# Kernel tuning notes

Hardware: AMD Instinct MI355X
Metric: run time of the kernel (lower is better)

Reference implementation:

```python
import jax, jax.numpy as jnp
import numpy as np

UNITS = 256
IN_DIM = 256
OUT_DIM = 10
TOL = 1e-4
MAX_ITER = 50


def setup_inputs() -> dict:
    key = jax.random.key(0)
    ks = jax.random.split(key, 16)
    B = 65536
    s = 1.0 / np.sqrt(UNITS)
    inp = {
        "x": jax.random.normal(ks[0], (B, IN_DIM), dtype=jnp.float32),
        "w_in": jax.random.normal(ks[1], (IN_DIM, UNITS), dtype=jnp.float32) * s,
        "b_in": jax.random.normal(ks[2], (UNITS,), dtype=jnp.float32) * 0.01,
        "w_out": jax.random.normal(ks[3], (UNITS, OUT_DIM), dtype=jnp.float32) * s,
        "b_out": jax.random.normal(ks[4], (OUT_DIM,), dtype=jnp.float32) * 0.01,
    }
    eye = jnp.eye(UNITS, dtype=jnp.float32)
    for i in range(4):
        # well-conditioned (invertible) implicit-layer weight: I + small perturbation
        inp[f"w{i+1}"] = eye + 0.1 * jax.random.normal(ks[5 + 2 * i], (UNITS, UNITS), dtype=jnp.float32) * s
        inp[f"b{i+1}"] = jax.random.normal(ks[6 + 2 * i], (UNITS,), dtype=jnp.float32) * 0.01
    return inp


def newton_block(x, W, b):
    # Solve z @ W = x + tanh(x) + b by Newton iteration with early exit on ||g||.
    c = x + jnp.tanh(x) + b  # [B, n]
    z0 = x
    g0 = z0 @ W - c

    def cond(state):
        z, g, it = state
        return (it < MAX_ITER) & (jnp.linalg.norm(g) >= TOL)

    def body(state):
        z, g, it = state
        # torch.solve(g[:, :, None], W^T.repeat(B,1,1)): shared matrix -> one solve
        z = z - jnp.linalg.solve(W.T, g.T).T
        g = z @ W - c
        return (z, g, it + 1)

    z, _, _ = jax.lax.while_loop(cond, body, (z0, g0, jnp.asarray(0)))
    z = jax.lax.stop_gradient(z)  # torch loop runs under no_grad
    # final differentiable correction (torch: z = z - (z@W - x - tanh(x) - b))
    return z - (z @ W - c)


def reference(x, w_in, b_in, w1, b1, w2, b2, w3, b3, w4, b4, w_out, b_out):
    z = x @ w_in + b_in
    z = newton_block(z, w1, b1)
    z = newton_block(z, w2, b2)
    z = newton_block(z, w3, b3)
    z = newton_block(z, w4, b4)
    logits = z @ w_out + b_out
    return jax.nn.softmax(logits, axis=1)
```

## Files before the change

kernel.cpp:

```cpp
#include <hip/hip_runtime.h>
#include <hip/hip_fp16.h>
#include <math.h>


typedef __attribute__((ext_vector_type(8))) short short8;
typedef __attribute__((ext_vector_type(4))) float f32x4;

__device__ __forceinline__ float tanh_fast(float x) {
#if __has_builtin(__builtin_amdgcn_exp2f)
  float e = __builtin_amdgcn_exp2f(x * 2.8853900817779268f);
#else
  float e = __expf(2.0f * x);
#endif
  return 1.0f - 2.0f * __builtin_amdgcn_rcpf(e + 1.0f);
}
__device__ __forceinline__ unsigned rn_pair16(float v0, float v1) {
  __half2 h = __floats2half2_rn(v0, v1);
  return *reinterpret_cast<unsigned*>(&h);
}
__device__ __forceinline__ unsigned rtz_pair16(float v0, float v1) {
#if __has_builtin(__builtin_amdgcn_cvt_pkrtz)
  typedef __fp16 h2v __attribute__((ext_vector_type(2)));
  h2v h = __builtin_amdgcn_cvt_pkrtz(v0, v1);
  return *reinterpret_cast<unsigned*>(&h);
#else
  return rn_pair16(v0, v1);
#endif
}

__global__ __launch_bounds__(256) void ns_poly_k(
    const float* __restrict__ w1, const float* __restrict__ w2,
    const float* __restrict__ w3, const float* __restrict__ w4,
    const float* __restrict__ w_in, const float* __restrict__ w_out,
    unsigned* __restrict__ pk) {
  const int bid = blockIdx.x;
  const int t = threadIdx.x;
  if (bid >= 256) {
    int idx = (bid - 256) * 256 + t;
    {
      int kc = idx >> 12;
      int nt = (idx >> 8) & 15;
      int lane = (idx >> 2) & 63;
      int d = idx & 3;
      int n = nt * 16 + (lane & 15);
      int kb = kc * 32 + (lane >> 4) * 8 + d * 2;
      pk[idx] = rn_pair16(w_in[kb * 256 + n], w_in[(kb + 1) * 256 + n]);
    }
    int idx2 = idx + 32768;
    if (idx2 < 34816) {
      int r2 = idx2 - 32768;
      int kc = r2 >> 8;
      int lane = (r2 >> 2) & 63;
      int d = r2 & 3;
      int n = lane & 15;
      int kb = kc * 32 + (lane >> 4) * 8 + d * 2;
      float v0 = (n < 10) ? w_out[kb * 10 + n] : 0.0f;
      float v1 = (n < 10) ? w_out[(kb + 1) * 10 + n] : 0.0f;
      pk[5 * 32768 + r2] = rn_pair16(v0, v1);
    }
    return;
  }
  const int m = bid >> 6;
  const int r0 = (bid & 63) * 4;
  const float* __restrict__ W = (m == 0) ? w1 : (m == 1) ? w2 : (m == 2) ? w3 : w4;
  __shared__ float S[4][256];

#pragma unroll
  for (int i = 0; i < 4; ++i) {
    int e = i * 256 + t;
    int r = e >> 8, c = e & 255;
    S[r][c] = (((r0 + r) == c) ? 6.0f : 0.0f) - W[(r0 + r) * 256 + c];
  }
  __syncthreads();

  const float coef[4] = {-15.0f, 20.0f, -15.0f, 6.0f};
#pragma unroll
  for (int step = 0; step < 4; ++step) {
    float acc[4];
#pragma unroll
    for (int r = 0; r < 4; ++r) acc[r] = 0.0f;
    for (int k = 0; k < 256; k += 4) {
      float4 sv[4];
#pragma unroll
      for (int r = 0; r < 4; ++r) sv[r] = *(const float4*)&S[r][k];
      float wv0 = W[(k + 0) * 256 + t];
      float wv1 = W[(k + 1) * 256 + t];
      float wv2 = W[(k + 2) * 256 + t];
      float wv3 = W[(k + 3) * 256 + t];
#pragma unroll
      for (int r = 0; r < 4; ++r) {
        acc[r] = fmaf(sv[r].x, wv0, acc[r]);
        acc[r] = fmaf(sv[r].y, wv1, acc[r]);
        acc[r] = fmaf(sv[r].z, wv2, acc[r]);
        acc[r] = fmaf(sv[r].w, wv3, acc[r]);
      }
    }
    __syncthreads();
    float cdiag = coef[step];
#pragma unroll
    for (int r = 0; r < 4; ++r)
      S[r][t] = acc[r] + (((r0 + r) == t) ? cdiag : 0.0f);
    __syncthreads();
  }

  const int kc = r0 >> 5;
  const int quad = (r0 >> 3) & 3;
  const int d0 = (r0 & 7) >> 1;
#pragma unroll
  for (int i = 0; i < 2; ++i) {
    int q = i * 256 + t;
    int nt = q >> 5;
    int n16 = (q >> 1) & 15;
    int dd = q & 1;
    int n = nt * 16 + n16;
    int lane = quad * 16 + n16;
    unsigned word = rn_pair16(S[2 * dd][n], S[2 * dd + 1][n]);
    pk[(m + 1) * 32768 + kc * 4096 + nt * 256 + lane * 4 + (d0 + dd)] = word;
  }
}

template <int MT>
__global__ __launch_bounds__(256, 4) void fused_k(
    const float* __restrict__ x, const unsigned* __restrict__ pk,
    const float* __restrict__ b_in,
    const float* __restrict__ b1, const float* __restrict__ b2,
    const float* __restrict__ b3, const float* __restrict__ b4,
    const float* __restrict__ b_out, float* __restrict__ out) {
  constexpr int NR = MT * 16;
  __shared__ unsigned short zpl[NR * 256];
  const int t = threadIdx.x;
  const int ln = t & 63;
  const int wv = t >> 6;
  const int quad = ln >> 4;
  const int n16 = ln & 15;
  const int grow0 = blockIdx.x * NR;

#pragma unroll
  for (int i = 0; i < MT * 4; ++i) {
    int e = i * 1024 + t * 4;
    int r = e >> 8, c = e & 255;
    float4 v = *(const float4*)(x + (grow0 + r) * 256 + c);
    int idx = r * 256 + (((c >> 3) ^ (r & 31)) * 8) + (c & 7);
    uint2 zp;
    zp.x = rtz_pair16(v.x, v.y);
    zp.y = rtz_pair16(v.z, v.w);
    *(uint2*)&zpl[idx] = zp;
  }
  __syncthreads();

  const float* bnv[4] = {b1, b2, b3, b4};
  f32x4 acc[MT][4];

  for (int layer = 0; layer < 5; ++layer) {
    const unsigned* pkl = pk + layer * 32768 + wv * 1024 + ln * 4;
#pragma unroll
    for (int mt = 0; mt < MT; ++mt)
#pragma unroll
      for (int nt = 0; nt < 4; ++nt) acc[mt][nt] = (f32x4){0.f, 0.f, 0.f, 0.f};

#pragma unroll 2
    for (int kc = 0; kc < 8; ++kc) {
      short8 wh[4], zf[MT];
      const unsigned* pb = pkl + kc * 4096;
#pragma unroll
      for (int nt = 0; nt < 4; ++nt) wh[nt] = *(const short8*)(pb + nt * 256);
#pragma unroll
      for (int mt = 0; mt < MT; ++mt) {
        int mm = mt * 16 + n16;
        int idx = mm * 256 + (((kc * 4 + quad) ^ (mm & 31)) * 8);
        zf[mt] = *(const short8*)&zpl[idx];
      }
#pragma unroll
      for (int mt = 0; mt < MT; ++mt)
#pragma unroll
        for (int nt = 0; nt < 4; ++nt)
          acc[mt][nt] = __builtin_amdgcn_mfma_f32_16x16x32_f16(wh[nt], zf[mt], acc[mt][nt], 0, 0, 0);
    }
    __syncthreads();

#pragma unroll
    for (int nt = 0; nt < 4; ++nt) {
      int colb = wv * 64 + nt * 16 + quad * 4;
      float4 bi = make_float4(0.f, 0.f, 0.f, 0.f);
      float4 bn4 = bi;
      if (layer == 0) bi = *(const float4*)(b_in + colb);
      if (layer < 4) bn4 = *(const float4*)(bnv[layer] + colb);
#pragma unroll
      for (int mt = 0; mt < MT; ++mt) {
        int row = mt * 16 + n16;
        float v0 = acc[mt][nt][0] + bi.x;
        float v1 = acc[mt][nt][1] + bi.y;
        float v2 = acc[mt][nt][2] + bi.z;
        float v3 = acc[mt][nt][3] + bi.w;
        if (layer < 4) {
          v0 = v0 + tanh_fast(v0) + bn4.x;
          v1 = v1 + tanh_fast(v1) + bn4.y;
          v2 = v2 + tanh_fast(v2) + bn4.z;
          v3 = v3 + tanh_fast(v3) + bn4.w;
        }
        int idx = row * 256 + (((colb >> 3) ^ (row & 31)) * 8) + (colb & 7);
        uint2 zp;
        zp.x = rtz_pair16(v0, v1);
        zp.y = rtz_pair16(v2, v3);
        *(uint2*)&zpl[idx] = zp;
      }
    }
    __syncthreads();
  }

  f32x4 lacc[MT];
#pragma unroll
  for (int mt = 0; mt < MT; ++mt) lacc[mt] = (f32x4){0.f, 0.f, 0.f, 0.f};
  const unsigned* pw = pk + 5 * 32768 + ln * 4;
#pragma unroll
  for (int kk = 0; kk < 2; ++kk) {
    int kc = wv * 2 + kk;
    short8 wh = *(const short8*)(pw + kc * 256);
#pragma unroll
    for (int mt = 0; mt < MT; ++mt) {
      int mm = mt * 16 + n16;
      int idx = mm * 256 + (((kc * 4 + quad) ^ (mm & 31)) * 8);
      short8 zf = *(const short8*)&zpl[idx];
      lacc[mt] = __builtin_amdgcn_mfma_f32_16x16x32_f16(wh, zf, lacc[mt], 0, 0, 0);
    }
  }
  __syncthreads();
  float* pbuf = (float*)zpl;
#pragma unroll
  for (int mt = 0; mt < MT; ++mt) {
    int addr = wv * (NR * 16) + (mt * 16 + n16) * 16 + quad * 4;
    *(f32x4*)&pbuf[addr] = lacc[mt];
  }
  __syncthreads();
  if (t < NR) {
    int r = t;
    float lg[10];
    float mx = -1e30f;
#pragma unroll
    for (int j = 0; j < 10; ++j) {
      float s = b_out[j];
#pragma unroll
      for (int w2 = 0; w2 < 4; ++w2) s += pbuf[w2 * (NR * 16) + r * 16 + j];
      lg[j] = s;
      mx = fmaxf(mx, s);
    }
    float sum = 0.f;
#pragma unroll
    for (int j = 0; j < 10; ++j) {
      lg[j] = __expf(lg[j] - mx);
      sum += lg[j];
    }
    float inv = 1.0f / sum;
    float* op = out + (grow0 + r) * 10;
#pragma unroll
    for (int j = 0; j < 10; ++j) op[j] = lg[j] * inv;
  }
}

extern "C" void kernel_launch(void* const* d_in, const int* in_sizes, int n_in,
                              void* d_out, int out_size, void* d_ws, size_t ws_size,
                              hipStream_t stream) {
  const float* x     = (const float*)d_in[0];
  const float* w_in  = (const float*)d_in[1];
  const float* b_in  = (const float*)d_in[2];
  const float* w_out = (const float*)d_in[3];
  const float* b_out = (const float*)d_in[4];
  const float* w1 = (const float*)d_in[5];
  const float* b1 = (const float*)d_in[6];
  const float* w2 = (const float*)d_in[7];
  const float* b2 = (const float*)d_in[8];
  const float* w3 = (const float*)d_in[9];
  const float* b3 = (const float*)d_in[10];
  const float* w4 = (const float*)d_in[11];
  const float* b4 = (const float*)d_in[12];
  float* out = (float*)d_out;

  unsigned* pk = (unsigned*)d_ws;

  ns_poly_k<<<384, 256, 0, stream>>>(w1, w2, w3, w4, w_in, w_out, pk);
  fused_k<4><<<1024, 256, 0, stream>>>(x, pk, b_in, b1, b2, b3, b4, b_out, out);
}
```

Before: 184.8 us.

## Restructure fused kernel into 1024-thread blocks with ping-pong MFMA/epilogue overlap

The fused kernel now uses 1024-thread blocks that each own 256 rows, split into four 64-row groups in shared memory. Each wave keeps its 16-column slice of the layer weights in registers (8 short8) instead of reloading weights every k-chunk. The work is software-pipelined: the tanh/bias epilogue of one row group is interleaved with the MFMA phase of the next, using two accumulator sets, so the matrix and vector units can overlap. Shared memory grows to 128 KB per block and there are fewer, larger blocks (256), which may reduce occupancy and raise register pressure.

Result: slower. 212.9 us (+15.2%).

```diff
diff --git a/kernel.cpp b/kernel.cpp
--- a/kernel.cpp
+++ b/kernel.cpp
@@ -119,141 +119,168 @@
   }
 }
 
-template <int MT>
-__global__ __launch_bounds__(256, 4) void fused_k(
+#define MFMA_PHASE(ACC, S)                                                     \
+  {                                                                            \
+    const unsigned short* pl = zpl + (S) * 16384;                              \
+    _Pragma("unroll") for (int mt = 0; mt < 4; ++mt)                           \
+        ACC[mt] = (f32x4){0.f, 0.f, 0.f, 0.f};                                 \
+    _Pragma("unroll") for (int kc = 0; kc < 8; ++kc) {                         \
+      short8 zf[4];                                                            \
+      _Pragma("unroll") for (int mt = 0; mt < 4; ++mt)                         \
+          zf[mt] = *(const short8*)&pl[rd_base[mt] + ((rd_pm[mt] ^ (kc * 4)) * 8)]; \
+      _Pragma("unroll") for (int mt = 0; mt < 4; ++mt)                         \
+          ACC[mt] = __builtin_amdgcn_mfma_f32_16x16x32_f16(wreg[kc], zf[mt],   \
+                                                           ACC[mt], 0, 0, 0); \
+    }                                                                          \
+  }
+
+#define EPI_PHASE(ACC, S, BN, BI, DOTANH)                                      \
+  {                                                                            \
+    unsigned short* pl = zpl + (S) * 16384;                                    \
+    float4 bn4 = make_float4(0.f, 0.f, 0.f, 0.f);                              \
+    float4 bi4 = make_float4(0.f, 0.f, 0.f, 0.f);                              \
+    if (DOTANH) bn4 = *(const float4*)((BN) + colb);                           \
+    if ((BI) != nullptr) bi4 = *(const float4*)((BI) + colb);                  \
+    _Pragma("unroll") for (int mt = 0; mt < 4; ++mt) {                         \
+      float v0 = ACC[mt][0] + bi4.x;                                           \
+      float v1 = ACC[mt][1] + bi4.y;                                           \
+      float v2 = ACC[mt][2] + bi4.z;                                           \
+      float v3 = ACC[mt][3] + bi4.w;                                           \
+      if (DOTANH) {                                                            \
+        v0 = v0 + tanh_fast(v0) + bn4.x;                                       \
+        v1 = v1 + tanh_fast(v1) + bn4.y;                                       \
+        v2 = v2 + tanh_fast(v2) + bn4.z;                                       \
+        v3 = v3 + tanh_fast(v3) + bn4.w;                                       \
+      }                                                                        \
+      uint2 zp;                                                                \
+      zp.x = rtz_pair16(v0, v1);                                               \
+      zp.y = rtz_pair16(v2, v3);                                               \
+      *(uint2*)&pl[wr_off[mt]] = zp;                                           \
+    }                                                                          \
+  }
+
+__global__ __launch_bounds__(1024, 4) void fused2_k(
     const float* __restrict__ x, const unsigned* __restrict__ pk,
     const float* __restrict__ b_in,
     const float* __restrict__ b1, const float* __restrict__ b2,
     const float* __restrict__ b3, const float* __restrict__ b4,
     const float* __restrict__ b_out, float* __restrict__ out) {
-  constexpr int NR = MT * 16;
-  __shared__ unsigned short zpl[NR * 256];
+  __shared__ unsigned short zpl[4 * 64 * 256];
   const int t = threadIdx.x;
   const int ln = t & 63;
   const int wv = t >> 6;
   const int quad = ln >> 4;
   const int n16 = ln & 15;
-  const int grow0 = blockIdx.x * NR;
-
-#pragma unroll
-  for (int i = 0; i < MT * 4; ++i) {
-    int e = i * 1024 + t * 4;
+  const int grow0 = blockIdx.x * 256;
+
+#pragma unroll
+  for (int i = 0; i < 16; ++i) {
+    int e = i * 4096 + t * 4;
     int r = e >> 8, c = e & 255;
     float4 v = *(const float4*)(x + (grow0 + r) * 256 + c);
-    int idx = r * 256 + (((c >> 3) ^ (r & 31)) * 8) + (c & 7);
+    int g = r >> 6, rl = r & 63;
+    int idx = g * 16384 + rl * 256 + (((c >> 3) ^ (rl & 31)) * 8) + (c & 7);
     uint2 zp;
     zp.x = rtz_pair16(v.x, v.y);
     zp.y = rtz_pair16(v.z, v.w);
     *(uint2*)&zpl[idx] = zp;
   }
+
+  const int colb = wv * 16 + quad * 4;
+  int rd_base[4], rd_pm[4], wr_off[4];
+#pragma unroll
+  for (int mt = 0; mt < 4; ++mt) {
+    int mm = mt * 16 + n16;
+    rd_base[mt] = mm * 256;
+    rd_pm[mt] = quad ^ (mm & 31);
+    wr_off[mt] = mm * 256 + (((colb >> 3) ^ (mm & 31)) * 8) + (colb & 7);
+  }
+
   __syncthreads();
 
-  const float* bnv[4] = {b1, b2, b3, b4};
-  f32x4 acc[MT][4];
+  f32x4 accA[4], accB[4];
 
   for (int layer = 0; layer < 5; ++layer) {
-    const unsigned* pkl = pk + layer * 32768 + wv * 1024 + ln * 4;
-#pragma unroll
-    for (int mt = 0; mt < MT; ++mt)
-#pragma unroll
-      for (int nt = 0; nt < 4; ++nt) acc[mt][nt] = (f32x4){0.f, 0.f, 0.f, 0.f};
-
-#pragma unroll 2
-    for (int kc = 0; kc < 8; ++kc) {
-      short8 wh[4], zf[MT];
-      const unsigned* pb = pkl + kc * 4096;
-#pragma unroll
-      for (int nt = 0; nt < 4; ++nt) wh[nt] = *(const short8*)(pb + nt * 256);
-#pragma unroll
-      for (int mt = 0; mt < MT; ++mt) {
-        int mm = mt * 16 + n16;
-        int idx = mm * 256 + (((kc * 4 + quad) ^ (mm & 31)) * 8);
-        zf[mt] = *(const short8*)&zpl[idx];
+    const unsigned* pkl = pk + layer * 32768 + wv * 256 + ln * 4;
+    short8 wreg[8];
+#pragma unroll
+    for (int kc = 0; kc < 8; ++kc) wreg[kc] = *(const short8*)(pkl + kc * 4096);
+
+    if (layer > 0) {
+      const float* bnp = (layer == 1) ? b1 : (layer == 2) ? b2 : (layer == 3) ? b3 : b4;
+      const float* bip = (layer == 1) ? b_in : nullptr;
+      EPI_PHASE(accB, 3, bnp, bip, true);
+    }
+    MFMA_PHASE(accA, 0);
+    __syncthreads();
+
+    const float* bn = (layer == 0) ? b1 : (layer == 1) ? b2 : (layer == 2) ? b3 : b4;
+    const float* bi0 = (layer == 0) ? b_in : nullptr;
+    const bool dt = (layer < 4);
+
+    EPI_PHASE(accA, 0, bn, bi0, dt);
+    MFMA_PHASE(accB, 1);
+    __syncthreads();
+    EPI_PHASE(accB, 1, bn, bi0, dt);
+    MFMA_PHASE(accA, 2);
+    __syncthreads();
+    EPI_PHASE(accA, 2, bn, bi0, dt);
+    MFMA_PHASE(accB, 3);
+    __syncthreads();
+  }
+  EPI_PHASE(accB, 3, (const float*)nullptr, (const float*)nullptr, false);
+  __syncthreads();
+
+  {
+    const int g = wv >> 2;
+    const int kw = wv & 3;
+    f32x4 lacc[4];
+#pragma unroll
+    for (int mt = 0; mt < 4; ++mt) lacc[mt] = (f32x4){0.f, 0.f, 0.f, 0.f};
+    const unsigned* pw = pk + 5 * 32768 + ln * 4;
+    const unsigned short* pl = zpl + g * 16384;
+#pragma unroll
+    for (int kk = 0; kk < 2; ++kk) {
+      int kc = kw * 2 + kk;
+      short8 wh = *(const short8*)(pw + kc * 256);
+#pragma unroll
+      for (int mt = 0; mt < 4; ++mt) {
+        short8 zf = *(const short8*)&pl[rd_base[mt] + ((rd_pm[mt] ^ (kc * 4)) * 8)];
+        lacc[mt] = __builtin_amdgcn_mfma_f32_16x16x32_f16(wh, zf, lacc[mt], 0, 0, 0);
       }
-#pragma unroll
-      for (int mt = 0; mt < MT; ++mt)
-#pragma unroll
-        for (int nt = 0; nt < 4; ++nt)
-          acc[mt][nt] = __builtin_amdgcn_mfma_f32_16x16x32_f16(wh[nt], zf[mt], acc[mt][nt], 0, 0, 0);
-    }
-    __syncthreads();
-
-#pragma unroll
-    for (int nt = 0; nt < 4; ++nt) {
-      int colb = wv * 64 + nt * 16 + quad * 4;
-      float4 bi = make_float4(0.f, 0.f, 0.f, 0.f);
-      float4 bn4 = bi;
-      if (layer == 0) bi = *(const float4*)(b_in + colb);
-      if (layer < 4) bn4 = *(const float4*)(bnv[layer] + colb);
-#pragma unroll
-      for (int mt = 0; mt < MT; ++mt) {
-        int row = mt * 16 + n16;
-        float v0 = acc[mt][nt][0] + bi.x;
-        float v1 = acc[mt][nt][1] + bi.y;
-        float v2 = acc[mt][nt][2] + bi.z;
-        float v3 = acc[mt][nt][3] + bi.w;
-        if (layer < 4) {
-          v0 = v0 + tanh_fast(v0) + bn4.x;
-          v1 = v1 + tanh_fast(v1) + bn4.y;
-          v2 = v2 + tanh_fast(v2) + bn4.z;
-          v3 = v3 + tanh_fast(v3) + bn4.w;
-        }
-        int idx = row * 256 + (((colb >> 3) ^ (row & 31)) * 8) + (colb & 7);
-        uint2 zp;
-        zp.x = rtz_pair16(v0, v1);
-        zp.y = rtz_pair16(v2, v3);
-        *(uint2*)&zpl[idx] = zp;
+    }
+    __syncthreads();
+    float* pbuf = (float*)zpl;
+#pragma unroll
+    for (int mt = 0; mt < 4; ++mt) {
+      int addr = g * 4096 + kw * 1024 + (mt * 16 + n16) * 16 + quad * 4;
+      *(f32x4*)&pbuf[addr] = lacc[mt];
+    }
+    __syncthreads();
+    if (t < 256) {
+      int g2 = t >> 6;
+      int rl = t & 63;
+      float lg[10];
+      float mx = -1e30f;
+#pragma unroll
+      for (int j = 0; j < 10; ++j) {
+        float s = b_out[j];
+#pragma unroll
+        for (int k2 = 0; k2 < 4; ++k2) s += pbuf[g2 * 4096 + k2 * 1024 + rl * 16 + j];
+        lg[j] = s;
+        mx = fmaxf(mx, s);
       }
-    }
-    __syncthreads();
-  }
-
-  f32x4 lacc[MT];
-#pragma unroll
-  for (int mt = 0; mt < MT; ++mt) lacc[mt] = (f32x4){0.f, 0.f, 0.f, 0.f};
-  const unsigned* pw = pk + 5 * 32768 + ln * 4;
-#pragma unroll
-  for (int kk = 0; kk < 2; ++kk) {
-    int kc = wv * 2 + kk;
-    short8 wh = *(const short8*)(pw + kc * 256);
-#pragma unroll
-    for (int mt = 0; mt < MT; ++mt) {
-      int mm = mt * 16 + n16;
-      int idx = mm * 256 + (((kc * 4 + quad) ^ (mm & 31)) * 8);
-      short8 zf = *(const short8*)&zpl[idx];
-      lacc[mt] = __builtin_amdgcn_mfma_f32_16x16x32_f16(wh, zf, lacc[mt], 0, 0, 0);
-    }
-  }
-  __syncthreads();
-  float* pbuf = (float*)zpl;
-#pragma unroll
-  for (int mt = 0; mt < MT; ++mt) {
-    int addr = wv * (NR * 16) + (mt * 16 + n16) * 16 + quad * 4;
-    *(f32x4*)&pbuf[addr] = lacc[mt];
-  }
-  __syncthreads();
-  if (t < NR) {
-    int r = t;
-    float lg[10];
-    float mx = -1e30f;
-#pragma unroll
-    for (int j = 0; j < 10; ++j) {
-      float s = b_out[j];
-#pragma unroll
-      for (int w2 = 0; w2 < 4; ++w2) s += pbuf[w2 * (NR * 16) + r * 16 + j];
-      lg[j] = s;
-      mx = fmaxf(mx, s);
-    }
-    float sum = 0.f;
-#pragma unroll
-    for (int j = 0; j < 10; ++j) {
-      lg[j] = __expf(lg[j] - mx);
-      sum += lg[j];
-    }
-    float inv = 1.0f / sum;
-    float* op = out + (grow0 + r) * 10;
-#pragma unroll
-    for (int j = 0; j < 10; ++j) op[j] = lg[j] * inv;
+      float sum = 0.f;
+#pragma unroll
+      for (int j = 0; j < 10; ++j) {
+        lg[j] = __expf(lg[j] - mx);
+        sum += lg[j];
+      }
+      float inv = 1.0f / sum;
+      float* op = out + (grow0 + t) * 10;
+#pragma unroll
+      for (int j = 0; j < 10; ++j) op[j] = lg[j] * inv;
+    }
   }
 }
 
@@ -278,5 +305,5 @@
   unsigned* pk = (unsigned*)d_ws;
 
   ns_poly_k<<<384, 256, 0, stream>>>(w1, w2, w3, w4, w_in, w_out, pk);
-  fused_k<4><<<1024, 256, 0, stream>>>(x, pk, b_in, b1, b2, b3, b4, b_out, out);
-}
+  fused2_k<<<256, 1024, 0, stream>>>(x, pk, b_in, b1, b2, b3, b4, b_out, out);
+}
```

## Double-buffer weight fragment loads across k-chunks and layers with MFMA priority

Applied to the files above, without the earlier changes.

Replaces the k-loop with a fully unrolled sequence that prefetches the next k-chunk's weight fragments into a second register buffer while MFMAs consume the current one. The first chunk of the next layer is also loaded before the epilogue and the initial x staging. Sched barriers pin the ordering, and s_setprio raises wave priority around the MFMA bursts. The goal is to hide global/L2 weight-load latency behind matrix math, at the cost of extra VGPRs under the 4-blocks-per-SM launch bound. The macros hardcode 4 m-tiles, so the code assumes MT==4.

Result: slower. 224.4 us (+21.5%).

```diff
diff --git a/kernel.cpp b/kernel.cpp
--- a/kernel.cpp
+++ b/kernel.cpp
@@ -119,6 +119,31 @@
   }
 }
 
+#define WLOAD(W, LAYER, KC)                                                    \
+  {                                                                            \
+    const unsigned* pb_ = pk + (LAYER) * 32768 + (KC) * 4096 + wv * 1024 + ln * 4; \
+    W[0] = *(const short8*)(pb_);                                              \
+    W[1] = *(const short8*)(pb_ + 256);                                        \
+    W[2] = *(const short8*)(pb_ + 512);                                        \
+    W[3] = *(const short8*)(pb_ + 768);                                        \
+  }
+
+#define STEP(W, KC)                                                            \
+  {                                                                            \
+    short8 zf[4];                                                              \
+    _Pragma("unroll") for (int mt = 0; mt < 4; ++mt) {                         \
+      int mm = mt * 16 + n16;                                                  \
+      zf[mt] = *(const short8*)&zpl[mm * 256 + ((((KC) * 4 + quad) ^ (mm & 31)) * 8)]; \
+    }                                                                          \
+    __builtin_amdgcn_s_setprio(1);                                             \
+    _Pragma("unroll") for (int mt = 0; mt < 4; ++mt)                           \
+      _Pragma("unroll") for (int nt = 0; nt < 4; ++nt)                         \
+        acc[mt][nt] = __builtin_amdgcn_mfma_f32_16x16x32_f16(                  \
+            W[nt], zf[mt], acc[mt][nt], 0, 0, 0);                              \
+    __builtin_amdgcn_s_setprio(0);                                             \
+  }
+#define SB __builtin_amdgcn_sched_barrier(0)
+
 template <int MT>
 __global__ __launch_bounds__(256, 4) void fused_k(
     const float* __restrict__ x, const unsigned* __restrict__ pk,
@@ -135,6 +160,9 @@
   const int n16 = ln & 15;
   const int grow0 = blockIdx.x * NR;
 
+  short8 whA[4], whB[4];
+  WLOAD(whA, 0, 0);
+
 #pragma unroll
   for (int i = 0; i < MT * 4; ++i) {
     int e = i * 1024 + t * 4;
@@ -152,31 +180,22 @@
   f32x4 acc[MT][4];
 
   for (int layer = 0; layer < 5; ++layer) {
-    const unsigned* pkl = pk + layer * 32768 + wv * 1024 + ln * 4;
 #pragma unroll
     for (int mt = 0; mt < MT; ++mt)
 #pragma unroll
       for (int nt = 0; nt < 4; ++nt) acc[mt][nt] = (f32x4){0.f, 0.f, 0.f, 0.f};
 
-#pragma unroll 2
-    for (int kc = 0; kc < 8; ++kc) {
-      short8 wh[4], zf[MT];
-      const unsigned* pb = pkl + kc * 4096;
-#pragma unroll
-      for (int nt = 0; nt < 4; ++nt) wh[nt] = *(const short8*)(pb + nt * 256);
-#pragma unroll
-      for (int mt = 0; mt < MT; ++mt) {
-        int mm = mt * 16 + n16;
-        int idx = mm * 256 + (((kc * 4 + quad) ^ (mm & 31)) * 8);
-        zf[mt] = *(const short8*)&zpl[idx];
-      }
-#pragma unroll
-      for (int mt = 0; mt < MT; ++mt)
-#pragma unroll
-        for (int nt = 0; nt < 4; ++nt)
-          acc[mt][nt] = __builtin_amdgcn_mfma_f32_16x16x32_f16(wh[nt], zf[mt], acc[mt][nt], 0, 0, 0);
-    }
+    WLOAD(whB, layer, 1); STEP(whA, 0); SB;
+    WLOAD(whA, layer, 2); STEP(whB, 1); SB;
+    WLOAD(whB, layer, 3); STEP(whA, 2); SB;
+    WLOAD(whA, layer, 4); STEP(whB, 3); SB;
+    WLOAD(whB, layer, 5); STEP(whA, 4); SB;
+    WLOAD(whA, layer, 6); STEP(whB, 5); SB;
+    WLOAD(whB, layer, 7); STEP(whA, 6); SB;
+    STEP(whB, 7);
     __syncthreads();
+
+    if (layer < 4) WLOAD(whA, layer + 1, 0);
 
 #pragma unroll
     for (int nt = 0; nt < 4; ++nt) {
```
